# Kernel tuning notes

Measured on AMD Instinct MI355X. Metric: run time of the kernel, lower is better.

## Reference

```python
import jax, jax.numpy as jnp
import numpy as np

HID = 128      # hidden_dim
NF = 128       # num_filters
NG = 50        # num_gaussians
NI = 3         # num_interactions
CUTOFF = 5.0
WIDTH = CUTOFF / NG  # GaussianSmearing width = (stop-start)/num_gaussians
B, N = 4, 512


def setup_inputs() -> dict:
    key = jax.random.key(0)
    ks = jax.random.split(key, 20)

    def lin_w(k, fan_in, shape):
        return (jax.random.normal(k, shape, jnp.float32) / np.float32(np.sqrt(fan_in)))

    positions = jax.random.uniform(ks[0], (B, N, 3), jnp.float32) * 10.0  # 10 A box
    node_indices = jax.random.randint(ks[1], (B, N), 1, 11)  # species ids, 0 = padding
    mask = jnp.ones((B, N), jnp.bool_)

    emb = jax.random.normal(ks[2], (11, HID), jnp.float32)
    emb = emb.at[0].set(0.0)  # padding_idx=0

    return dict(
        positions=positions,
        emb=emb,
        rbf_w1=lin_w(ks[3], NG, (NI, NG, NF)),
        rbf_b1=jnp.zeros((NI, NF), jnp.float32),
        rbf_w2=lin_w(ks[4], NF, (NI, NF, NF)),
        rbf_b2=jnp.zeros((NI, NF), jnp.float32),
        f_w=lin_w(ks[5], HID, (NI, HID, NF)),
        f_b=jnp.zeros((NI, NF), jnp.float32),
        out_w1=lin_w(ks[6], NF, (NI, NF, HID)),
        out_b1=jnp.zeros((NI, HID), jnp.float32),
        out_w2=lin_w(ks[7], HID, (NI, HID, HID)),
        out_b2=jnp.zeros((NI, HID), jnp.float32),
        atom_w1=lin_w(ks[8], HID, (HID, HID)),
        atom_b1=jnp.zeros((HID,), jnp.float32),
        atom_w2=lin_w(ks[9], HID, (HID, 1)),
        atom_b2=jnp.zeros((1,), jnp.float32),
        node_indices=node_indices,
        mask=mask,
    )


def _forward(positions, emb, rbf_w1, rbf_b1, rbf_w2, rbf_b2, f_w, f_b,
             out_w1, out_b1, out_w2, out_b2, atom_w1, atom_b1, atom_w2, atom_b2,
             node_indices, mask):
    sp = jax.nn.softplus
    mask = mask.astype(jnp.bool_)
    maskf = mask.astype(positions.dtype)

    # pairwise distances with safe sqrt (zero grad on diagonal)
    disp = positions[:, :, None, :] - positions[:, None, :, :]        # (B,N,N,3)
    sq = jnp.sum(disp * disp, axis=-1)                                # (B,N,N)
    dist = jnp.sqrt(jnp.where(sq > 0, sq, 1.0))
    dist = jnp.where(sq > 0, dist, 0.0)

    nmask = mask[:, None, :] & mask[:, :, None]                       # valid pairs
    nmask = nmask & (dist <= CUTOFF)                                  # cutoff (adjacency=None)
    n = positions.shape[1]
    nmask = nmask & ~jnp.eye(n, dtype=jnp.bool_)[None]                # no self-loops
    nm = nmask[..., None].astype(positions.dtype)

    offset = jnp.linspace(0.0, CUTOFF, NG).astype(positions.dtype)
    rbf = jnp.exp(-0.5 * ((dist[..., None] - offset) / WIDTH) ** 2) * nm  # (B,N,N,NG)

    feats = emb[node_indices]                                         # (B,N,HID)
    for i in range(NI):
        # filter-generating MLP on pair features: (B,N,N,NG) -> (B,N,N,NF)
        filt = sp(jnp.einsum('bijg,gf->bijf', rbf, rbf_w1[i]) + rbf_b1[i])
        filt = jnp.einsum('bijf,fk->bijk', filt, rbf_w2[i]) + rbf_b2[i]
        nf = feats @ f_w[i] + f_b[i]                                  # (B,N,NF)
        # messages = filt * nf[:,None] masked; sum over neighbour axis j
        agg = jnp.einsum('bijf,bjf->bif', filt * nm, nf)              # (B,N,NF)
        feats = feats + (sp(agg @ out_w1[i] + out_b1[i]) @ out_w2[i] + out_b2[i])

    per_atom = (sp(feats @ atom_w1 + atom_b1) @ atom_w2 + atom_b2)[..., 0] * maskf
    return per_atom.sum(axis=1)                                        # energy (B,)


def reference(positions, emb, rbf_w1, rbf_b1, rbf_w2, rbf_b2, f_w, f_b,
              out_w1, out_b1, out_w2, out_b2, atom_w1, atom_b1, atom_w2, atom_b2,
              node_indices, mask):
    return _forward(positions, emb, rbf_w1, rbf_b1, rbf_w2, rbf_b2, f_w, f_b,
                    out_w1, out_b1, out_w2, out_b2, atom_w1, atom_b1, atom_w2,
                    atom_b2, node_indices, mask)
```

## Files before the change

kernel.cpp:

```cpp
#include <hip/hip_runtime.h>
#include <math.h>


#define HID 128
#define NF_ 128
#define NG_ 50
#define NI_ 3
#define NK_ 1024
#define NB_ 4
#define NN_ 512
#define GA8 8
#define GPRE 4
#define GAT 4
#define NATOM (NB_ * NN_)
#define TBLK (NI_ * (NK_ / GA8))

typedef unsigned int uint32;
typedef unsigned short ushort16;

static __device__ __forceinline__ float softplus_f(float x) {
    return fmaxf(x, 0.0f) + log1pf(expf(-fabsf(x)));
}

static __device__ __forceinline__ ushort16 f2bf(float x) {
    uint32 b = __float_as_uint(x);
    uint32 r = b + 0x7FFFu + ((b >> 16) & 1u);
    return (ushort16)(r >> 16);
}

template <int G>
static __device__ __forceinline__ void gemv_half(const float (*src)[HID],
                                                 const float* __restrict__ w,
                                                 int f, int kh, float* acc) {
    int cb = kh * 64;
#pragma unroll
    for (int u = 0; u < G; ++u) acc[u] = 0.0f;
#pragma unroll 2
    for (int c0 = 0; c0 < 64; c0 += 8) {
        float wv[8];
#pragma unroll
        for (int q = 0; q < 8; ++q) wv[q] = w[(cb + c0 + q) * NF_ + f];
#pragma unroll
        for (int u = 0; u < G; ++u) {
            const float4 x0 = *(const float4*)&src[u][cb + c0];
            const float4 x1 = *(const float4*)&src[u][cb + c0 + 4];
            acc[u] = fmaf(x0.x, wv[0], acc[u]);
            acc[u] = fmaf(x0.y, wv[1], acc[u]);
            acc[u] = fmaf(x0.z, wv[2], acc[u]);
            acc[u] = fmaf(x0.w, wv[3], acc[u]);
            acc[u] = fmaf(x1.x, wv[4], acc[u]);
            acc[u] = fmaf(x1.y, wv[5], acc[u]);
            acc[u] = fmaf(x1.z, wv[6], acc[u]);
            acc[u] = fmaf(x1.w, wv[7], acc[u]);
        }
    }
}

__global__ __launch_bounds__(256, 4)
void k_prep(const float* __restrict__ w1all, const float* __restrict__ b1all,
            const float* __restrict__ w2all, const float* __restrict__ b2all,
            const float* __restrict__ emb, const int* __restrict__ nidx,
            const float* __restrict__ fw, const float* __restrict__ fb,
            ushort16* __restrict__ tabU, float* __restrict__ feats,
            ushort16* __restrict__ nf, float* __restrict__ out) {
    __shared__ float smem[3472];
    int tid = threadIdx.x;
    int f = tid & 127, kh = tid >> 7;

    if (blockIdx.x < TBLK) {
        int it = blockIdx.x >> 7;
        int k0 = (blockIdx.x & 127) * GA8;
        const float* w1 = w1all + (size_t)it * NG_ * NF_;
        const float* b1 = b1all + (size_t)it * NF_;
        const float* w2 = w2all + (size_t)it * NF_ * NF_;
        const float* b2 = b2all + (size_t)it * NF_;
        ushort16* tu = tabU + (size_t)it * NK_ * NF_ * 2;

        float (*rbf)[NG_] = (float (*)[NG_])smem;
        float (*s_h)[HID] = (float (*)[HID])(smem + 400);
        float (*s_p)[GA8][HID] = (float (*)[GA8][HID])(smem + 1424);

        for (int idx = tid; idx < GA8 * NG_; idx += 256) {
            int u = idx / NG_, g = idx - u * NG_;
            float d = (float)(k0 + u) * (5.0f / (float)(NK_ - 1));
            float off = (float)g * (5.0f / (float)(NG_ - 1));
            float z = (d - off) * 10.0f;
            rbf[u][g] = expf(-0.5f * z * z);
        }
        __syncthreads();
        float acc[GA8];
#pragma unroll
        for (int u = 0; u < GA8; ++u) acc[u] = 0.0f;
        int gb = kh * 25;
#pragma unroll 1
        for (int g0 = 0; g0 < 25; g0 += 5) {
            float wv[5];
#pragma unroll
            for (int qq = 0; qq < 5; ++qq) wv[qq] = w1[(gb + g0 + qq) * NF_ + f];
#pragma unroll
            for (int u = 0; u < GA8; ++u)
#pragma unroll
                for (int qq = 0; qq < 5; ++qq)
                    acc[u] = fmaf(rbf[u][gb + g0 + qq], wv[qq], acc[u]);
        }
#pragma unroll
        for (int u = 0; u < GA8; ++u) s_p[kh][u][f] = acc[u];
        __syncthreads();
        if (kh == 0) {
#pragma unroll
            for (int u = 0; u < GA8; ++u)
                s_h[u][f] = softplus_f(s_p[0][u][f] + s_p[1][u][f] + b1[f]);
        }
        __syncthreads();
        gemv_half<GA8>(s_h, w2, f, kh, acc);
#pragma unroll
        for (int u = 0; u < GA8; ++u) s_p[kh][u][f] = acc[u];
        __syncthreads();
        if (kh == 0) {
#pragma unroll
            for (int u = 0; u < GA8; ++u) {
                int k = k0 + u;
                ushort16 v = f2bf(s_p[0][u][f] + s_p[1][u][f] + b2[f]);
                tu[((size_t)k * NF_ + f) * 2] = v;
                if (k > 0) tu[((size_t)(k - 1) * NF_ + f) * 2 + 1] = v;
            }
        }
    } else {
        int a0 = (blockIdx.x - TBLK) * GPRE;
        if (blockIdx.x == TBLK && tid < NB_) out[tid] = 0.0f;
        float (*s_x)[HID] = (float (*)[HID])smem;
        float (*s_p)[GPRE][HID] = (float (*)[GPRE][HID])(smem + 512);
        for (int idx2 = tid; idx2 < GPRE * HID; idx2 += 256) {
            int u = idx2 >> 7, c = idx2 & 127;
            float v = emb[nidx[a0 + u] * HID + c];
            s_x[u][c] = v;
            feats[(size_t)(a0 + u) * HID + c] = v;
        }
        __syncthreads();
        float acc[GPRE];
        gemv_half<GPRE>(s_x, fw, f, kh, acc);
#pragma unroll
        for (int u = 0; u < GPRE; ++u) s_p[kh][u][f] = acc[u];
        __syncthreads();
        if (kh == 0) {
#pragma unroll
            for (int u = 0; u < GPRE; ++u)
                nf[(size_t)(a0 + u) * NF_ + f] =
                    f2bf(s_p[0][u][f] + s_p[1][u][f] + fb[f]);
        }
    }
}

static __device__ __forceinline__ void gemv_q4(const float (*src)[HID],
                                               const float* __restrict__ w,
                                               int f, int q, float* acc) {
    int cb = q * 32;
#pragma unroll
    for (int u = 0; u < GAT; ++u) acc[u] = 0.0f;
#pragma unroll
    for (int c0 = 0; c0 < 32; c0 += 8) {
        float wv[8];
#pragma unroll
        for (int qq = 0; qq < 8; ++qq) wv[qq] = w[(cb + c0 + qq) * NF_ + f];
#pragma unroll
        for (int u = 0; u < GAT; ++u) {
            const float4 x0 = *(const float4*)&src[u][cb + c0];
            const float4 x1 = *(const float4*)&src[u][cb + c0 + 4];
            acc[u] = fmaf(x0.x, wv[0], acc[u]);
            acc[u] = fmaf(x0.y, wv[1], acc[u]);
            acc[u] = fmaf(x0.z, wv[2], acc[u]);
            acc[u] = fmaf(x0.w, wv[3], acc[u]);
            acc[u] = fmaf(x1.x, wv[4], acc[u]);
            acc[u] = fmaf(x1.y, wv[5], acc[u]);
            acc[u] = fmaf(x1.z, wv[6], acc[u]);
            acc[u] = fmaf(x1.w, wv[7], acc[u]);
        }
    }
}

static __device__ __forceinline__ void agg_phase(
        const float* __restrict__ posB, const ushort16* __restrict__ nfB,
        const uint32* __restrict__ tab, int a0, int tid,
        int (*s_jk)[NN_], float (*s_t)[NN_], int (*s_wc)[8],
        float2 (*s_p8)[GAT][64], float (*s_x)[HID]) {
    int lane = tid & 63;
    int wave = tid >> 6;
    float pxj = posB[tid * 3 + 0];
    float pyj = posB[tid * 3 + 1];
    float pzj = posB[tid * 3 + 2];

    bool  vals[GAT];
    int   kks[GAT];
    float frs[GAT];
#pragma unroll
    for (int u = 0; u < GAT; ++u) {
        int i = (a0 + u) & (NN_ - 1);
        float dx = pxj - posB[i * 3 + 0];
        float dy = pyj - posB[i * 3 + 1];
        float dz = pzj - posB[i * 3 + 2];
        float sq = dx * dx + dy * dy + dz * dz;
        float d = sqrtf(sq);
        bool valid = (tid != i) && (d <= 5.0f);
        float x = d * ((float)(NK_ - 1) / 5.0f);
        int kk = (int)x;
        if (kk > NK_ - 2) kk = NK_ - 2;
        vals[u] = valid;
        kks[u] = kk;
        frs[u] = x - (float)kk;
        unsigned long long m = __ballot(valid);
        if (lane == 0) s_wc[u][wave] = (int)__popcll(m);
    }
    __syncthreads();
    int cnts[GAT];
#pragma unroll
    for (int u = 0; u < GAT; ++u) {
        unsigned long long m = __ballot(vals[u]);
        int base = (int)__popcll(m & ((1ull << lane) - 1ull));
        int cnt = 0;
#pragma unroll
        for (int w = 0; w < 8; ++w) {
            int c = s_wc[u][w];
            if (wave > w) base += c;
            cnt += c;
        }
        cnts[u] = cnt;
        if (vals[u]) {
            s_jk[u][base] = (kks[u] << 9) | tid;
            s_t[u][base] = frs[u];
        }
    }
    __syncthreads();

    int f2 = lane;
    int fo = 2 * f2;
#pragma unroll
    for (int u = 0; u < GAT; ++u) {
        int cnt = cnts[u];
        float ax0 = 0.0f, ay0 = 0.0f, ax1 = 0.0f, ay1 = 0.0f;
        int e = wave;
        for (; e + 8 < cnt; e += 16) {
            int jk0 = s_jk[u][e], jk1 = s_jk[u][e + 8];
            float t0 = s_t[u][e], t1 = s_t[u][e + 8];
            const uint2 w0 = *(const uint2*)&tab[((jk0 >> 9) << 7) + fo];
            const uint2 w1 = *(const uint2*)&tab[((jk1 >> 9) << 7) + fo];
            uint32 nv0 = *(const uint32*)&nfB[((jk0 & 511) << 7) + fo];
            uint32 nv1 = *(const uint32*)&nfB[((jk1 & 511) << 7) + fo];
            float n0x = __uint_as_float(nv0 << 16);
            float n0y = __uint_as_float(nv0 & 0xFFFF0000u);
            float n1x = __uint_as_float(nv1 << 16);
            float n1y = __uint_as_float(nv1 & 0xFFFF0000u);
            float p0x = __uint_as_float(w0.x << 16);
            float q0x = __uint_as_float(w0.x & 0xFFFF0000u);
            float p0y = __uint_as_float(w0.y << 16);
            float q0y = __uint_as_float(w0.y & 0xFFFF0000u);
            float p1x = __uint_as_float(w1.x << 16);
            float q1x = __uint_as_float(w1.x & 0xFFFF0000u);
            float p1y = __uint_as_float(w1.y << 16);
            float q1y = __uint_as_float(w1.y & 0xFFFF0000u);
            ax0 = fmaf(fmaf(t0, q0x - p0x, p0x), n0x, ax0);
            ay0 = fmaf(fmaf(t0, q0y - p0y, p0y), n0y, ay0);
            ax1 = fmaf(fmaf(t1, q1x - p1x, p1x), n1x, ax1);
            ay1 = fmaf(fmaf(t1, q1y - p1y, p1y), n1y, ay1);
        }
        if (e < cnt) {
            int jk0 = s_jk[u][e];
            float t0 = s_t[u][e];
            const uint2 w0 = *(const uint2*)&tab[((jk0 >> 9) << 7) + fo];
            uint32 nv0 = *(const uint32*)&nfB[((jk0 & 511) << 7) + fo];
            float n0x = __uint_as_float(nv0 << 16);
            float n0y = __uint_as_float(nv0 & 0xFFFF0000u);
            float p0x = __uint_as_float(w0.x << 16);
            float q0x = __uint_as_float(w0.x & 0xFFFF0000u);
            float p0y = __uint_as_float(w0.y << 16);
            float q0y = __uint_as_float(w0.y & 0xFFFF0000u);
            ax0 = fmaf(fmaf(t0, q0x - p0x, p0x), n0x, ax0);
            ay0 = fmaf(fmaf(t0, q0y - p0y, p0y), n0y, ay0);
        }
        s_p8[wave][u][f2] = make_float2(ax0 + ax1, ay0 + ay1);
    }
    __syncthreads();
    {
        int u = tid >> 7, f = tid & 127;
        const float* pp = (const float*)&s_p8[0][u][0] + f;
        float s = 0.0f;
#pragma unroll
        for (int g = 0; g < 8; ++g) s += pp[(size_t)g * GAT * 128];
        s_x[u][f] = s;
    }
    __syncthreads();
}

__global__ __launch_bounds__(512, 8)
void k_fused(const float* __restrict__ positions,
             const ushort16* __restrict__ nf_in,
             const uint32* __restrict__ tab,
             const float* __restrict__ w1, const float* __restrict__ b1,
             const float* __restrict__ w2, const float* __restrict__ b2,
             const float* __restrict__ fw, const float* __restrict__ fb,
             float* __restrict__ feats, ushort16* __restrict__ nf_out) {
    int a0 = blockIdx.x * GAT;
    int b = a0 >> 9;
    int tid = threadIdx.x;
    int f = tid & 127, q = tid >> 7;
    const float* posB = positions + (size_t)b * NN_ * 3;
    const ushort16* nfB = nf_in + (size_t)b * NN_ * NF_;

    __shared__ int    s_jk[GAT][NN_];
    __shared__ float  s_t[GAT][NN_];
    __shared__ int    s_wc[GAT][8];
    __shared__ float2 s_p8[8][GAT][64];
    __shared__ float  s_x[GAT][HID];
    __shared__ float  s_h[GAT][HID];

    agg_phase(posB, nfB, tab, a0, tid, s_jk, s_t, s_wc, s_p8, s_x);

    float acc[GAT];
    float (*s_pq)[GAT][HID] = (float (*)[GAT][HID])s_p8;
    gemv_q4(s_x, w1, f, q, acc);
#pragma unroll
    for (int u = 0; u < GAT; ++u) s_pq[q][u][f] = acc[u];
    __syncthreads();
    s_h[q][f] = softplus_f(s_pq[0][q][f] + s_pq[1][q][f] + s_pq[2][q][f]
                           + s_pq[3][q][f] + b1[f]);
    __syncthreads();
    gemv_q4(s_h, w2, f, q, acc);
#pragma unroll
    for (int u = 0; u < GAT; ++u) s_pq[q][u][f] = acc[u];
    __syncthreads();
    {
        float v = feats[(size_t)(a0 + q) * HID + f]
                + s_pq[0][q][f] + s_pq[1][q][f] + s_pq[2][q][f] + s_pq[3][q][f]
                + b2[f];
        feats[(size_t)(a0 + q) * HID + f] = v;
        s_x[q][f] = v;
    }
    __syncthreads();
    gemv_q4(s_x, fw, f, q, acc);
#pragma unroll
    for (int u = 0; u < GAT; ++u) s_pq[q][u][f] = acc[u];
    __syncthreads();
    nf_out[(size_t)(a0 + q) * NF_ + f] =
        f2bf(s_pq[0][q][f] + s_pq[1][q][f] + s_pq[2][q][f] + s_pq[3][q][f] + fb[f]);
}

__global__ __launch_bounds__(512, 8)
void k_fused_final(const float* __restrict__ positions,
                   const ushort16* __restrict__ nf_in,
                   const uint32* __restrict__ tab,
                   const float* __restrict__ w1, const float* __restrict__ b1,
                   const float* __restrict__ w2, const float* __restrict__ b2,
                   const float* __restrict__ aw1, const float* __restrict__ ab1,
                   const float* __restrict__ aw2, const float* __restrict__ ab2,
                   const float* __restrict__ feats, float* __restrict__ out) {
    int a0 = blockIdx.x * GAT;
    int b = a0 >> 9;
    int tid = threadIdx.x;
    int f = tid & 127, q = tid >> 7;
    const float* posB = positions + (size_t)b * NN_ * 3;
    const ushort16* nfB = nf_in + (size_t)b * NN_ * NF_;

    __shared__ int    s_jk[GAT][NN_];
    __shared__ float  s_t[GAT][NN_];
    __shared__ int    s_wc[GAT][8];
    __shared__ float2 s_p8[8][GAT][64];
    __shared__ float  s_x[GAT][HID];
    __shared__ float  s_h[GAT][HID];
    __shared__ float  red[128];

    agg_phase(posB, nfB, tab, a0, tid, s_jk, s_t, s_wc, s_p8, s_x);

    float acc[GAT];
    float (*s_pq)[GAT][HID] = (float (*)[GAT][HID])s_p8;
    gemv_q4(s_x, w1, f, q, acc);
#pragma unroll
    for (int u = 0; u < GAT; ++u) s_pq[q][u][f] = acc[u];
    __syncthreads();
    s_h[q][f] = softplus_f(s_pq[0][q][f] + s_pq[1][q][f] + s_pq[2][q][f]
                           + s_pq[3][q][f] + b1[f]);
    __syncthreads();
    gemv_q4(s_h, w2, f, q, acc);
#pragma unroll
    for (int u = 0; u < GAT; ++u) s_pq[q][u][f] = acc[u];
    __syncthreads();
    s_x[q][f] = feats[(size_t)(a0 + q) * HID + f]
              + s_pq[0][q][f] + s_pq[1][q][f] + s_pq[2][q][f] + s_pq[3][q][f]
              + b2[f];
    __syncthreads();
    gemv_q4(s_x, aw1, f, q, acc);
#pragma unroll
    for (int u = 0; u < GAT; ++u) s_pq[q][u][f] = acc[u];
    __syncthreads();
    s_h[q][f] = softplus_f(s_pq[0][q][f] + s_pq[1][q][f] + s_pq[2][q][f]
                           + s_pq[3][q][f] + ab1[f]) * aw2[f];
    __syncthreads();
    if (tid < 128)
        red[tid] = (s_h[0][tid] + s_h[1][tid]) + (s_h[2][tid] + s_h[3][tid]);
    __syncthreads();
    for (int s = 64; s > 0; s >>= 1) {
        if (tid < s) red[tid] += red[tid + s];
        __syncthreads();
    }
    if (tid == 0) atomicAdd(&out[b], red[0] + (float)GAT * ab2[0]);
}

extern "C" void kernel_launch(void* const* d_in, const int* in_sizes, int n_in,
                              void* d_out, int out_size, void* d_ws, size_t ws_size,
                              hipStream_t stream) {
    const float* positions = (const float*)d_in[0];
    const float* emb       = (const float*)d_in[1];
    const float* rbf_w1    = (const float*)d_in[2];
    const float* rbf_b1    = (const float*)d_in[3];
    const float* rbf_w2    = (const float*)d_in[4];
    const float* rbf_b2    = (const float*)d_in[5];
    const float* f_w       = (const float*)d_in[6];
    const float* f_b       = (const float*)d_in[7];
    const float* out_w1    = (const float*)d_in[8];
    const float* out_b1    = (const float*)d_in[9];
    const float* out_w2    = (const float*)d_in[10];
    const float* out_b2    = (const float*)d_in[11];
    const float* atom_w1   = (const float*)d_in[12];
    const float* atom_b1   = (const float*)d_in[13];
    const float* atom_w2   = (const float*)d_in[14];
    const float* atom_b2   = (const float*)d_in[15];
    const int*   node_idx  = (const int*)d_in[16];

    float* out = (float*)d_out;
    float* ws = (float*)d_ws;

    float*    feats = ws;
    ushort16* nf0   = (ushort16*)(ws + 262144);
    ushort16* nf1   = (ushort16*)(ws + 393216);
    uint32*   tab   = (uint32*)(ws + 524288);

    k_prep<<<TBLK + NATOM / GPRE, 256, 0, stream>>>(rbf_w1, rbf_b1, rbf_w2, rbf_b2,
                                                    emb, node_idx, f_w, f_b,
                                                    (ushort16*)tab, feats, nf0, out);

    ushort16* nfs[2] = { nf0, nf1 };
    for (int it = 0; it < NI_ - 1; ++it) {
        k_fused<<<NATOM / GAT, 512, 0, stream>>>(
            positions, nfs[it & 1], tab + (size_t)it * NK_ * NF_,
            out_w1 + (size_t)it * NF_ * HID, out_b1 + (size_t)it * HID,
            out_w2 + (size_t)it * HID * HID, out_b2 + (size_t)it * HID,
            f_w + (size_t)(it + 1) * HID * NF_, f_b + (size_t)(it + 1) * NF_,
            feats, nfs[(it + 1) & 1]);
    }
    k_fused_final<<<NATOM / GAT, 512, 0, stream>>>(
        positions, nfs[(NI_ - 1) & 1], tab + (size_t)(NI_ - 1) * NK_ * NF_,
        out_w1 + (size_t)(NI_ - 1) * NF_ * HID, out_b1 + (size_t)(NI_ - 1) * HID,
        out_w2 + (size_t)(NI_ - 1) * HID * HID, out_b2 + (size_t)(NI_ - 1) * HID,
        atom_w1, atom_b1, atom_w2, atom_b2,
        feats, out);
}
```

Measured before the change: 92.78 us.

## Split fused interaction kernel into separate neighbour-aggregation and update kernels

Each interaction is now two kernels instead of one fused kernel. The first does neighbour aggregation over twice as many blocks, each covering half of the j range. It uses wider loads per thread: 4 features of the filter table and 2 packed nf words at once. Its partial sums go to a global buffer, and a separate update kernel adds the two halves and runs the MLP GEMVs. This raises parallelism and memory-level parallelism in the gather phase, at the cost of extra kernel launches and a global round trip for the aggregation results.

```diff
diff --git a/kernel.cpp b/kernel.cpp
--- a/kernel.cpp
+++ b/kernel.cpp
@@ -151,6 +151,150 @@
     }
 }
 
+__global__ __launch_bounds__(512, 8)
+void k_agg(const float* __restrict__ positions,
+           const ushort16* __restrict__ nf_in,
+           const uint32* __restrict__ tab,
+           float* __restrict__ aggbuf) {
+    int ab = blockIdx.x >> 1;
+    int jh = blockIdx.x & 1;
+    int a0 = ab * GAT;
+    int b = a0 >> 9;
+    int tid = threadIdx.x;
+    int lane = tid & 63;
+    int wave = tid >> 6;
+    const float* posB = positions + (size_t)b * NN_ * 3;
+    const uint32* nfU = (const uint32*)(nf_in + (size_t)b * NN_ * NF_);
+
+    __shared__ int    s_jk[GAT][256];
+    __shared__ float  s_t[GAT][256];
+    __shared__ int    s_wc[GAT][4];
+    __shared__ float4 s_p[2][8][2][32];
+
+    bool  vals[GAT];
+    int   kks[GAT];
+    float frs[GAT];
+    if (tid < 256) {
+        int j = jh * 256 + tid;
+        float pxj = posB[j * 3 + 0];
+        float pyj = posB[j * 3 + 1];
+        float pzj = posB[j * 3 + 2];
+#pragma unroll
+        for (int u = 0; u < GAT; ++u) {
+            int i = (a0 + u) & (NN_ - 1);
+            float dx = pxj - posB[i * 3 + 0];
+            float dy = pyj - posB[i * 3 + 1];
+            float dz = pzj - posB[i * 3 + 2];
+            float sq = dx * dx + dy * dy + dz * dz;
+            float d = sqrtf(sq);
+            bool valid = (j != i) && (d <= 5.0f);
+            float x = d * ((float)(NK_ - 1) / 5.0f);
+            int kk = (int)x;
+            if (kk > NK_ - 2) kk = NK_ - 2;
+            vals[u] = valid;
+            kks[u] = kk;
+            frs[u] = x - (float)kk;
+            unsigned long long m = __ballot(valid);
+            if (lane == 0) s_wc[u][wave] = (int)__popcll(m);
+        }
+    }
+    __syncthreads();
+    int cnts[GAT];
+#pragma unroll
+    for (int u = 0; u < GAT; ++u)
+        cnts[u] = s_wc[u][0] + s_wc[u][1] + s_wc[u][2] + s_wc[u][3];
+    if (tid < 256) {
+        int j = jh * 256 + tid;
+#pragma unroll
+        for (int u = 0; u < GAT; ++u) {
+            unsigned long long m = __ballot(vals[u]);
+            int base = (int)__popcll(m & ((1ull << lane) - 1ull));
+#pragma unroll
+            for (int w = 0; w < 4; ++w)
+                if (wave > w) base += s_wc[u][w];
+            if (vals[u]) {
+                s_jk[u][base] = (kks[u] << 9) | j;
+                s_t[u][base] = frs[u];
+            }
+        }
+    }
+    __syncthreads();
+
+    int half = tid >> 8;
+    int g = (tid >> 5) & 7;
+    int f4 = tid & 31;
+    int tfo = 4 * f4;
+    int nfo = 2 * f4;
+#pragma unroll
+    for (int uu = 0; uu < 2; ++uu) {
+        int u = half * 2 + uu;
+        int cnt = cnts[u];
+        float ax = 0.0f, ay = 0.0f, az = 0.0f, aw = 0.0f;
+        float bx = 0.0f, by = 0.0f, bz = 0.0f, bw = 0.0f;
+        int e = g;
+        for (; e + 8 < cnt; e += 16) {
+            int jk0 = s_jk[u][e], jk1 = s_jk[u][e + 8];
+            float t0 = s_t[u][e], t1 = s_t[u][e + 8];
+            const uint4 w0 = *(const uint4*)&tab[((jk0 >> 9) << 7) + tfo];
+            const uint4 w1 = *(const uint4*)&tab[((jk1 >> 9) << 7) + tfo];
+            const uint2 n0 = *(const uint2*)&nfU[((jk0 & 511) << 6) + nfo];
+            const uint2 n1 = *(const uint2*)&nfU[((jk1 & 511) << 6) + nfo];
+            {
+                float p0 = __uint_as_float(w0.x << 16), q0 = __uint_as_float(w0.x & 0xFFFF0000u);
+                float p1 = __uint_as_float(w0.y << 16), q1 = __uint_as_float(w0.y & 0xFFFF0000u);
+                float p2 = __uint_as_float(w0.z << 16), q2 = __uint_as_float(w0.z & 0xFFFF0000u);
+                float p3 = __uint_as_float(w0.w << 16), q3 = __uint_as_float(w0.w & 0xFFFF0000u);
+                float m0 = __uint_as_float(n0.x << 16), m1 = __uint_as_float(n0.x & 0xFFFF0000u);
+                float m2 = __uint_as_float(n0.y << 16), m3 = __uint_as_float(n0.y & 0xFFFF0000u);
+                ax = fmaf(fmaf(t0, q0 - p0, p0), m0, ax);
+                ay = fmaf(fmaf(t0, q1 - p1, p1), m1, ay);
+                az = fmaf(fmaf(t0, q2 - p2, p2), m2, az);
+                aw = fmaf(fmaf(t0, q3 - p3, p3), m3, aw);
+            }
+            {
+                float p0 = __uint_as_float(w1.x << 16), q0 = __uint_as_float(w1.x & 0xFFFF0000u);
+                float p1 = __uint_as_float(w1.y << 16), q1 = __uint_as_float(w1.y & 0xFFFF0000u);
+                float p2 = __uint_as_float(w1.z << 16), q2 = __uint_as_float(w1.z & 0xFFFF0000u);
+                float p3 = __uint_as_float(w1.w << 16), q3 = __uint_as_float(w1.w & 0xFFFF0000u);
+                float m0 = __uint_as_float(n1.x << 16), m1 = __uint_as_float(n1.x & 0xFFFF0000u);
+                float m2 = __uint_as_float(n1.y << 16), m3 = __uint_as_float(n1.y & 0xFFFF0000u);
+                bx = fmaf(fmaf(t1, q0 - p0, p0), m0, bx);
+                by = fmaf(fmaf(t1, q1 - p1, p1), m1, by);
+                bz = fmaf(fmaf(t1, q2 - p2, p2), m2, bz);
+                bw = fmaf(fmaf(t1, q3 - p3, p3), m3, bw);
+            }
+        }
+        if (e < cnt) {
+            int jk0 = s_jk[u][e];
+            float t0 = s_t[u][e];
+            const uint4 w0 = *(const uint4*)&tab[((jk0 >> 9) << 7) + tfo];
+            const uint2 n0 = *(const uint2*)&nfU[((jk0 & 511) << 6) + nfo];
+            float p0 = __uint_as_float(w0.x << 16), q0 = __uint_as_float(w0.x & 0xFFFF0000u);
+            float p1 = __uint_as_float(w0.y << 16), q1 = __uint_as_float(w0.y & 0xFFFF0000u);
+            float p2 = __uint_as_float(w0.z << 16), q2 = __uint_as_float(w0.z & 0xFFFF0000u);
+            float p3 = __uint_as_float(w0.w << 16), q3 = __uint_as_float(w0.w & 0xFFFF0000u);
+            float m0 = __uint_as_float(n0.x << 16), m1 = __uint_as_float(n0.x & 0xFFFF0000u);
+            float m2 = __uint_as_float(n0.y << 16), m3 = __uint_as_float(n0.y & 0xFFFF0000u);
+            ax = fmaf(fmaf(t0, q0 - p0, p0), m0, ax);
+            ay = fmaf(fmaf(t0, q1 - p1, p1), m1, ay);
+            az = fmaf(fmaf(t0, q2 - p2, p2), m2, az);
+            aw = fmaf(fmaf(t0, q3 - p3, p3), m3, aw);
+        }
+        s_p[half][g][uu][f4] = make_float4(ax + bx, ay + by, az + bz, aw + bw);
+    }
+    __syncthreads();
+
+    {
+        int u = tid >> 7, f = tid & 127;
+        int fq = f >> 2, c = f & 3;
+        const float* pp = (const float*)&s_p[u >> 1][0][u & 1][fq] + c;
+        float s = 0.0f;
+#pragma unroll
+        for (int gg = 0; gg < 8; ++gg) s += pp[(size_t)gg * 2 * 32 * 4];
+        aggbuf[(size_t)jh * NATOM * NF_ + (size_t)(a0 + u) * NF_ + f] = s;
+    }
+}
+
 static __device__ __forceinline__ void gemv_q4(const float (*src)[HID],
                                                const float* __restrict__ w,
                                                int f, int q, float* acc) {
@@ -178,144 +322,23 @@
     }
 }
 
-static __device__ __forceinline__ void agg_phase(
-        const float* __restrict__ posB, const ushort16* __restrict__ nfB,
-        const uint32* __restrict__ tab, int a0, int tid,
-        int (*s_jk)[NN_], float (*s_t)[NN_], int (*s_wc)[8],
-        float2 (*s_p8)[GAT][64], float (*s_x)[HID]) {
-    int lane = tid & 63;
-    int wave = tid >> 6;
-    float pxj = posB[tid * 3 + 0];
-    float pyj = posB[tid * 3 + 1];
-    float pzj = posB[tid * 3 + 2];
-
-    bool  vals[GAT];
-    int   kks[GAT];
-    float frs[GAT];
-#pragma unroll
-    for (int u = 0; u < GAT; ++u) {
-        int i = (a0 + u) & (NN_ - 1);
-        float dx = pxj - posB[i * 3 + 0];
-        float dy = pyj - posB[i * 3 + 1];
-        float dz = pzj - posB[i * 3 + 2];
-        float sq = dx * dx + dy * dy + dz * dz;
-        float d = sqrtf(sq);
-        bool valid = (tid != i) && (d <= 5.0f);
-        float x = d * ((float)(NK_ - 1) / 5.0f);
-        int kk = (int)x;
-        if (kk > NK_ - 2) kk = NK_ - 2;
-        vals[u] = valid;
-        kks[u] = kk;
-        frs[u] = x - (float)kk;
-        unsigned long long m = __ballot(valid);
-        if (lane == 0) s_wc[u][wave] = (int)__popcll(m);
-    }
-    __syncthreads();
-    int cnts[GAT];
-#pragma unroll
-    for (int u = 0; u < GAT; ++u) {
-        unsigned long long m = __ballot(vals[u]);
-        int base = (int)__popcll(m & ((1ull << lane) - 1ull));
-        int cnt = 0;
-#pragma unroll
-        for (int w = 0; w < 8; ++w) {
-            int c = s_wc[u][w];
-            if (wave > w) base += c;
-            cnt += c;
-        }
-        cnts[u] = cnt;
-        if (vals[u]) {
-            s_jk[u][base] = (kks[u] << 9) | tid;
-            s_t[u][base] = frs[u];
-        }
-    }
-    __syncthreads();
-
-    int f2 = lane;
-    int fo = 2 * f2;
-#pragma unroll
-    for (int u = 0; u < GAT; ++u) {
-        int cnt = cnts[u];
-        float ax0 = 0.0f, ay0 = 0.0f, ax1 = 0.0f, ay1 = 0.0f;
-        int e = wave;
-        for (; e + 8 < cnt; e += 16) {
-            int jk0 = s_jk[u][e], jk1 = s_jk[u][e + 8];
-            float t0 = s_t[u][e], t1 = s_t[u][e + 8];
-            const uint2 w0 = *(const uint2*)&tab[((jk0 >> 9) << 7) + fo];
-            const uint2 w1 = *(const uint2*)&tab[((jk1 >> 9) << 7) + fo];
-            uint32 nv0 = *(const uint32*)&nfB[((jk0 & 511) << 7) + fo];
-            uint32 nv1 = *(const uint32*)&nfB[((jk1 & 511) << 7) + fo];
-            float n0x = __uint_as_float(nv0 << 16);
-            float n0y = __uint_as_float(nv0 & 0xFFFF0000u);
-            float n1x = __uint_as_float(nv1 << 16);
-            float n1y = __uint_as_float(nv1 & 0xFFFF0000u);
-            float p0x = __uint_as_float(w0.x << 16);
-            float q0x = __uint_as_float(w0.x & 0xFFFF0000u);
-            float p0y = __uint_as_float(w0.y << 16);
-            float q0y = __uint_as_float(w0.y & 0xFFFF0000u);
-            float p1x = __uint_as_float(w1.x << 16);
-            float q1x = __uint_as_float(w1.x & 0xFFFF0000u);
-            float p1y = __uint_as_float(w1.y << 16);
-            float q1y = __uint_as_float(w1.y & 0xFFFF0000u);
-            ax0 = fmaf(fmaf(t0, q0x - p0x, p0x), n0x, ax0);
-            ay0 = fmaf(fmaf(t0, q0y - p0y, p0y), n0y, ay0);
-            ax1 = fmaf(fmaf(t1, q1x - p1x, p1x), n1x, ax1);
-            ay1 = fmaf(fmaf(t1, q1y - p1y, p1y), n1y, ay1);
-        }
-        if (e < cnt) {
-            int jk0 = s_jk[u][e];
-            float t0 = s_t[u][e];
-            const uint2 w0 = *(const uint2*)&tab[((jk0 >> 9) << 7) + fo];
-            uint32 nv0 = *(const uint32*)&nfB[((jk0 & 511) << 7) + fo];
-            float n0x = __uint_as_float(nv0 << 16);
-            float n0y = __uint_as_float(nv0 & 0xFFFF0000u);
-            float p0x = __uint_as_float(w0.x << 16);
-            float q0x = __uint_as_float(w0.x & 0xFFFF0000u);
-            float p0y = __uint_as_float(w0.y << 16);
-            float q0y = __uint_as_float(w0.y & 0xFFFF0000u);
-            ax0 = fmaf(fmaf(t0, q0x - p0x, p0x), n0x, ax0);
-            ay0 = fmaf(fmaf(t0, q0y - p0y, p0y), n0y, ay0);
-        }
-        s_p8[wave][u][f2] = make_float2(ax0 + ax1, ay0 + ay1);
-    }
-    __syncthreads();
-    {
-        int u = tid >> 7, f = tid & 127;
-        const float* pp = (const float*)&s_p8[0][u][0] + f;
-        float s = 0.0f;
-#pragma unroll
-        for (int g = 0; g < 8; ++g) s += pp[(size_t)g * GAT * 128];
-        s_x[u][f] = s;
-    }
-    __syncthreads();
-}
-
 __global__ __launch_bounds__(512, 8)
-void k_fused(const float* __restrict__ positions,
-             const ushort16* __restrict__ nf_in,
-             const uint32* __restrict__ tab,
-             const float* __restrict__ w1, const float* __restrict__ b1,
-             const float* __restrict__ w2, const float* __restrict__ b2,
-             const float* __restrict__ fw, const float* __restrict__ fb,
-             float* __restrict__ feats, ushort16* __restrict__ nf_out) {
+void k_upd(const float* __restrict__ aggbuf,
+           const float* __restrict__ w1, const float* __restrict__ b1,
+           const float* __restrict__ w2, const float* __restrict__ b2,
+           const float* __restrict__ fw, const float* __restrict__ fb,
+           float* __restrict__ feats, ushort16* __restrict__ nf_out) {
     int a0 = blockIdx.x * GAT;
-    int b = a0 >> 9;
     int tid = threadIdx.x;
     int f = tid & 127, q = tid >> 7;
-    const float* posB = positions + (size_t)b * NN_ * 3;
-    const ushort16* nfB = nf_in + (size_t)b * NN_ * NF_;
-
-    __shared__ int    s_jk[GAT][NN_];
-    __shared__ float  s_t[GAT][NN_];
-    __shared__ int    s_wc[GAT][8];
-    __shared__ float2 s_p8[8][GAT][64];
-    __shared__ float  s_x[GAT][HID];
-    __shared__ float  s_h[GAT][HID];
-
-    agg_phase(posB, nfB, tab, a0, tid, s_jk, s_t, s_wc, s_p8, s_x);
-
+    __shared__ float s_x[GAT][HID];
+    __shared__ float s_h[GAT][HID];
+    __shared__ float s_pq[4][GAT][HID];
+
+    s_x[q][f] = aggbuf[(size_t)(a0 + q) * NF_ + f]
+              + aggbuf[(size_t)NATOM * NF_ + (size_t)(a0 + q) * NF_ + f];
+    __syncthreads();
     float acc[GAT];
-    float (*s_pq)[GAT][HID] = (float (*)[GAT][HID])s_p8;
     gemv_q4(s_x, w1, f, q, acc);
 #pragma unroll
     for (int u = 0; u < GAT; ++u) s_pq[q][u][f] = acc[u];
@@ -344,33 +367,25 @@
 }
 
 __global__ __launch_bounds__(512, 8)
-void k_fused_final(const float* __restrict__ positions,
-                   const ushort16* __restrict__ nf_in,
-                   const uint32* __restrict__ tab,
-                   const float* __restrict__ w1, const float* __restrict__ b1,
-                   const float* __restrict__ w2, const float* __restrict__ b2,
-                   const float* __restrict__ aw1, const float* __restrict__ ab1,
-                   const float* __restrict__ aw2, const float* __restrict__ ab2,
-                   const float* __restrict__ feats, float* __restrict__ out) {
+void k_upd_final(const float* __restrict__ aggbuf,
+                 const float* __restrict__ w1, const float* __restrict__ b1,
+                 const float* __restrict__ w2, const float* __restrict__ b2,
+                 const float* __restrict__ aw1, const float* __restrict__ ab1,
+                 const float* __restrict__ aw2, const float* __restrict__ ab2,
+                 const float* __restrict__ feats, float* __restrict__ out) {
     int a0 = blockIdx.x * GAT;
     int b = a0 >> 9;
     int tid = threadIdx.x;
     int f = tid & 127, q = tid >> 7;
-    const float* posB = positions + (size_t)b * NN_ * 3;
-    const ushort16* nfB = nf_in + (size_t)b * NN_ * NF_;
-
-    __shared__ int    s_jk[GAT][NN_];
-    __shared__ float  s_t[GAT][NN_];
-    __shared__ int    s_wc[GAT][8];
-    __shared__ float2 s_p8[8][GAT][64];
-    __shared__ float  s_x[GAT][HID];
-    __shared__ float  s_h[GAT][HID];
-    __shared__ float  red[128];
-
-    agg_phase(posB, nfB, tab, a0, tid, s_jk, s_t, s_wc, s_p8, s_x);
-
+    __shared__ float s_x[GAT][HID];
+    __shared__ float s_h[GAT][HID];
+    __shared__ float s_pq[4][GAT][HID];
+    __shared__ float red[128];
+
+    s_x[q][f] = aggbuf[(size_t)(a0 + q) * NF_ + f]
+              + aggbuf[(size_t)NATOM * NF_ + (size_t)(a0 + q) * NF_ + f];
+    __syncthreads();
     float acc[GAT];
-    float (*s_pq)[GAT][HID] = (float (*)[GAT][HID])s_p8;
     gemv_q4(s_x, w1, f, q, acc);
 #pragma unroll
     for (int u = 0; u < GAT; ++u) s_pq[q][u][f] = acc[u];
@@ -427,28 +442,34 @@
     float* out = (float*)d_out;
     float* ws = (float*)d_ws;
 
-    float*    feats = ws;
-    ushort16* nf0   = (ushort16*)(ws + 262144);
-    ushort16* nf1   = (ushort16*)(ws + 393216);
-    uint32*   tab   = (uint32*)(ws + 524288);
+    float*    feats  = ws;
+    ushort16* nf0    = (ushort16*)(ws + 262144);
+    ushort16* nf1    = (ushort16*)(ws + 393216);
+    uint32*   tab    = (uint32*)(ws + 524288);
+    float*    aggbuf = ws + 917504;
 
     k_prep<<<TBLK + NATOM / GPRE, 256, 0, stream>>>(rbf_w1, rbf_b1, rbf_w2, rbf_b2,
                                                     emb, node_idx, f_w, f_b,
                                                     (ushort16*)tab, feats, nf0, out);
 
     ushort16* nfs[2] = { nf0, nf1 };
-    for (int it = 0; it < NI_ - 1; ++it) {
-        k_fused<<<NATOM / GAT, 512, 0, stream>>>(
-            positions, nfs[it & 1], tab + (size_t)it * NK_ * NF_,
-            out_w1 + (size_t)it * NF_ * HID, out_b1 + (size_t)it * HID,
-            out_w2 + (size_t)it * HID * HID, out_b2 + (size_t)it * HID,
-            f_w + (size_t)(it + 1) * HID * NF_, f_b + (size_t)(it + 1) * NF_,
-            feats, nfs[(it + 1) & 1]);
-    }
-    k_fused_final<<<NATOM / GAT, 512, 0, stream>>>(
-        positions, nfs[(NI_ - 1) & 1], tab + (size_t)(NI_ - 1) * NK_ * NF_,
-        out_w1 + (size_t)(NI_ - 1) * NF_ * HID, out_b1 + (size_t)(NI_ - 1) * HID,
-        out_w2 + (size_t)(NI_ - 1) * HID * HID, out_b2 + (size_t)(NI_ - 1) * HID,
-        atom_w1, atom_b1, atom_w2, atom_b2,
-        feats, out);
-}
+    for (int it = 0; it < NI_; ++it) {
+        k_agg<<<(NATOM / GAT) * 2, 512, 0, stream>>>(
+            positions, nfs[it & 1], tab + (size_t)it * NK_ * NF_, aggbuf);
+        if (it < NI_ - 1) {
+            k_upd<<<NATOM / GAT, 512, 0, stream>>>(
+                aggbuf,
+                out_w1 + (size_t)it * NF_ * HID, out_b1 + (size_t)it * HID,
+                out_w2 + (size_t)it * HID * HID, out_b2 + (size_t)it * HID,
+                f_w + (size_t)(it + 1) * HID * NF_, f_b + (size_t)(it + 1) * NF_,
+                feats, nfs[(it + 1) & 1]);
+        } else {
+            k_upd_final<<<NATOM / GAT, 512, 0, stream>>>(
+                aggbuf,
+                out_w1 + (size_t)it * NF_ * HID, out_b1 + (size_t)it * HID,
+                out_w2 + (size_t)it * HID * HID, out_b2 + (size_t)it * HID,
+                atom_w1, atom_b1, atom_w2, atom_b2,
+                feats, out);
+        }
+    }
+}
```

Result: faster. 90.55 us (-2.4%).
